# Kernel optimization log

Hardware: AMD Instinct MI355X
Metric: run time of the kernel (lower is better)

Reference implementation:

```python
import jax, jax.numpy as jnp
import numpy as np

DIM = 128      # d_msa
HEADS = 8
DH = 64        # dim_head
INNER = HEADS * DH  # 512
R = 64         # tie_attn_dim (MSA rows)
N = 512        # residues
DPAIR = 128
LN_EPS = 1e-5


def _layernorm(x, g, b):
    mu = jnp.mean(x, axis=-1, keepdims=True)
    var = jnp.mean((x - mu) ** 2, axis=-1, keepdims=True)
    return (x - mu) * jax.lax.rsqrt(var + LN_EPS) * g + b


def setup_inputs() -> dict:
    key = jax.random.key(0)
    ks = jax.random.split(key, 12)
    s = 0.02
    return {
        "x": jax.random.normal(ks[0], (R, N, DIM), jnp.float32),
        "pair_bias": jax.random.normal(ks[1], (1, N, N, DPAIR), jnp.float32),
        "Wq": jax.random.normal(ks[2], (DIM, INNER), jnp.float32) * s,
        "Wkv": jax.random.normal(ks[3], (DIM, 2 * INNER), jnp.float32) * s,
        "Wo": jax.random.normal(ks[4], (INNER, DIM), jnp.float32) * s,
        "bo": jnp.zeros((DIM,), jnp.float32),
        "ln_g": jnp.ones((DPAIR,), jnp.float32),
        "ln_b": jnp.zeros((DPAIR,), jnp.float32),
        "Wpair": jax.random.normal(ks[5], (DPAIR, HEADS), jnp.float32) * s,
        "Wsq": jax.random.normal(ks[6], (DIM, DIM), jnp.float32) * s,
        "bsq": jnp.zeros((DIM,), jnp.float32),
        "Wsk": jax.random.normal(ks[7], (DIM, DIM), jnp.float32) * s,
        "bsk": jnp.zeros((DIM,), jnp.float32),
        "tie_attn_dim": R,
    }


def reference(x, pair_bias, Wq, Wkv, Wo, bo, ln_g, ln_b, Wpair, Wsq, bsq, Wsk, bsk, tie_attn_dim):
    r = tie_attn_dim
    br, n, dim = x.shape
    b = br // r
    h, dh = HEADS, DH
    dsw = dim // h  # per-head dim inside PositionalWiseWeight

    # projections: (b*r, n, inner) -> (b, r, h, n, dh)
    q = (x @ Wq).reshape(b, r, n, h, dh).transpose(0, 1, 3, 2, 4)
    kv = x @ Wkv
    k, v = jnp.split(kv, 2, axis=-1)
    k = k.reshape(b, r, n, h, dh).transpose(0, 1, 3, 2, 4)
    v = v.reshape(b, r, n, h, dh).transpose(0, 1, 3, 2, 4)

    # soft tied row weights (PositionalWiseWeight): w[b, i(pos), h, r]
    m = x.reshape(b, r, n, dim)
    sq = (m[:, :1] @ Wsq + bsq).reshape(b, 1, n, h, dsw).transpose(0, 2, 3, 1, 4)  # b n h 1 d
    sk = (m @ Wsk + bsk).reshape(b, r, n, h, dsw).transpose(0, 2, 3, 1, 4)          # b n h r d
    wlog = jnp.einsum('bnhud,bnhrd->bnhr', sq, sk) / np.float32(np.sqrt(dsw))
    w = jax.nn.softmax(wlog, axis=-1)  # softmax over rows r

    # tied-row attention logits with soft weights
    scale = np.float32(dh) ** -0.5
    dots = jnp.einsum('bihr,brhid,brhjd->bhij', w, q, k) * scale

    # pair bias: LayerNorm + Linear(dim_pair -> heads), broadcast into logits
    pb = _layernorm(pair_bias, ln_g, ln_b) @ Wpair  # (b, i, j, h)
    dots = dots + pb.transpose(0, 3, 1, 2)

    attn = jax.nn.softmax(dots, axis=-1)  # (b, h, i, j)

    out = jnp.einsum('bhij,brhjd->brhid', attn, v)           # (b, r, h, n, dh)
    out = out.transpose(0, 1, 3, 2, 4).reshape(br, n, h * dh)
    out = out @ Wo + bo                                       # (b*r, n, dim)
    return out.reshape(1, br, n, dim)
```

## Files before the change

### kernel.cpp

```cpp
#include <hip/hip_runtime.h>
#include <hip/hip_bf16.h>

typedef unsigned short u16;
typedef unsigned int u32;
typedef __attribute__((ext_vector_type(8))) short short8;
typedef __attribute__((ext_vector_type(4))) float floatx4;

__device__ inline float bf2f(u16 u) { union { u32 i; float f; } v; v.i = ((u32)u) << 16; return v.f; }
__device__ inline u16 f2bf(float f) {
    union { float f; u32 i; } v; v.f = f;
    u32 lsb = (v.i >> 16) & 1u;
    v.i += 0x7fffu + lsb;
    return (u16)(v.i >> 16);
}

__device__ inline uint4 pack8(float4 a, float4 b) {
    uint4 q;
    q.x = (u32)f2bf(a.x) | ((u32)f2bf(a.y) << 16);
    q.y = (u32)f2bf(a.z) | ((u32)f2bf(a.w) << 16);
    q.z = (u32)f2bf(b.x) | ((u32)f2bf(b.y) << 16);
    q.w = (u32)f2bf(b.z) | ((u32)f2bf(b.w) << 16);
    return q;
}

__device__ inline void ld8(u16* dst, const float* src) {
    const float4 a = *(const float4*)src;
    const float4 b = *(const float4*)(src + 4);
    *(uint4*)dst = pack8(a, b);
}

__device__ inline void async16(u16* ldst, const u16* gsrc) {
    __builtin_amdgcn_global_load_lds((const __attribute__((address_space(1))) u32*)gsrc,
                                     (__attribute__((address_space(3))) u32*)ldst, 16, 0, 0);
}

template <int N> __device__ inline void waitvm() {
    static_assert(N == 0 || N == 3 || N == 4 || N == 6 || N == 8, "unsupported vmcnt");
    if constexpr (N == 0) asm volatile("s_waitcnt vmcnt(0)" ::: "memory");
    if constexpr (N == 3) asm volatile("s_waitcnt vmcnt(3)" ::: "memory");
    if constexpr (N == 4) asm volatile("s_waitcnt vmcnt(4)" ::: "memory");
    if constexpr (N == 6) asm volatile("s_waitcnt vmcnt(6)" ::: "memory");
    if constexpr (N == 8) asm volatile("s_waitcnt vmcnt(8)" ::: "memory");
}
__device__ inline void barrier_raw() {
    asm volatile("s_barrier" ::: "memory");
    __builtin_amdgcn_sched_barrier(0);
}
__device__ inline void waitlgkm0() {
    asm volatile("s_waitcnt lgkmcnt(0)" ::: "memory");
    __builtin_amdgcn_sched_barrier(0);
}

template <int BM, int BN, class Epi>
__global__ __launch_bounds__(256) void gemm_nt(const u16* __restrict__ A, const u16* __restrict__ B,
                                               long sAz, long sBz, int lda, int ldb, int K, int zlog, Epi epi)
{
    constexpr int AELE = BM * 32, BELE = BN * 32;
    constexpr int SLOT = AELE + BELE;
    constexpr int IA = BM / 64, IB = BN / 64;
    constexpr int PW = IA + IB;
    constexpr bool STAGE = Epi::chunked;
    static_assert(!STAGE || BN == 128, "chunked epilogue assumes BN=128");
    constexpr int LDC = BN + 4;
    constexpr size_t RB = sizeof(u16) * 4 * (size_t)SLOT;
    constexpr size_t EBR = STAGE ? sizeof(float) * 64 * (size_t)LDC : 0;
    constexpr size_t EBV = (STAGE && Epi::kv) ? sizeof(float) * 128 * 68 : 0;
    constexpr size_t EB = EBR > EBV ? EBR : EBV;
    constexpr size_t LB = RB > EB ? RB : EB;
    __shared__ __align__(16) char smem[LB];
    u16* lds = (u16*)smem;
    const int tid  = threadIdx.x;
    const int lane = tid & 63;
    const int wave = tid >> 6;
    const int z    = blockIdx.z;
    const int zh   = z >> zlog;
    const int zk   = z & ((1 << zlog) - 1);
    if constexpr (Epi::ylim >= 0) {
        if (zh != 0 && (int)blockIdx.y >= Epi::ylim) return;
    }
    const long row0 = (long)blockIdx.y * BM;
    const long col0 = (long)blockIdx.x * BN;
    const u16* Ab = A + (long)zh * sAz + row0 * lda + (long)zk * K;
    const u16* Bb = B + (long)zh * sBz + col0 * ldb + (long)zk * K;
    constexpr int WM = BM / 2, WN = BN / 2, TM = WM / 16, TN = WN / 16;
    const int wm = (wave >> 1) * WM;
    const int wn = (wave & 1) * WN;
    const int l15 = lane & 15;
    const int quad = lane >> 4;
    const int swz = (l15 >> 1) & 3;

    floatx4 acc[TM][TN];
#pragma unroll
    for (int i = 0; i < TM; i++)
#pragma unroll
        for (int j = 0; j < TN; j++) acc[i][j] = (floatx4){0.f, 0.f, 0.f, 0.f};

    auto stage = [&](int slot, int ki) {
        const int k0 = ki << 5;
        u16* base = lds + slot * SLOT;
#pragma unroll
        for (int i2 = 0; i2 < IA; i2++) {
            int s = wave * (IA * 64) + i2 * 64 + lane;
            int r = s >> 2, c = (s & 3) ^ ((r >> 1) & 3);
            async16(base + (wave * (IA * 64) + i2 * 64) * 8, Ab + (long)r * lda + k0 + c * 8);
        }
        u16* bbase = base + AELE;
#pragma unroll
        for (int i2 = 0; i2 < IB; i2++) {
            int s = wave * (IB * 64) + i2 * 64 + lane;
            int r = s >> 2, c = (s & 3) ^ ((r >> 1) & 3);
            async16(bbase + (wave * (IB * 64) + i2 * 64) * 8, Bb + (long)r * ldb + k0 + c * 8);
        }
    };

    auto compute = [&](int slot) {
        const u16* As = lds + slot * SLOT;
        const u16* Bs = As + AELE;
        short8 af[TM], bfr[TN];
#pragma unroll
        for (int t = 0; t < TM; t++)
            af[t] = *(const short8*)(As + (wm + t * 16 + l15) * 32 + (quad ^ swz) * 8);
#pragma unroll
        for (int t = 0; t < TN; t++)
            bfr[t] = *(const short8*)(Bs + (wn + t * 16 + l15) * 32 + (quad ^ swz) * 8);
        waitlgkm0();
#pragma unroll
        for (int i = 0; i < TM; i++)
#pragma unroll
            for (int j = 0; j < TN; j++)
                acc[i][j] = __builtin_amdgcn_mfma_f32_16x16x32_bf16(af[i], bfr[j], acc[i][j], 0, 0, 0);
    };

    const int nIter = K >> 5;
    stage(0, 0);
    stage(1, 1);
    for (int i = 0; i + 2 < nIter; i++) {
        stage((i + 2) & 3, i + 2);
        waitvm<2 * PW>();
        barrier_raw();
        compute(i & 3);
    }
    waitvm<PW>(); barrier_raw(); compute((nIter - 2) & 3);
    waitvm<0>();  barrier_raw(); compute((nIter - 1) & 3);

    if constexpr (STAGE) {
        float* cs = (float*)smem;
        constexpr int NP = BM / 64;
        bool vtile = false;
        if constexpr (Epi::kv) vtile = (col0 >= 512);
#pragma unroll
        for (int p = 0; p < NP; p++) {
            __syncthreads();
            if (!vtile) {
                if ((wm >> 6) == p) {
                    const int lr0 = wm & 63;
#pragma unroll
                    for (int i = 0; i < TM; i++)
#pragma unroll
                        for (int j = 0; j < TN; j++)
#pragma unroll
                            for (int r = 0; r < 4; r++)
                                cs[(lr0 + i * 16 + quad * 4 + r) * LDC + wn + j * 16 + l15] = acc[i][j][r];
                }
                __syncthreads();
                constexpr int CPT = (64 * BN) / (256 * 8);
#pragma unroll
                for (int k = 0; k < CPT; k++) {
                    int g = k * 256 + tid;
                    int row = g >> 4, c8 = (g & 15) * 8;
                    const float* pp = cs + row * LDC + c8;
                    float4 a = *(const float4*)pp;
                    float4 b = *(const float4*)(pp + 4);
                    epi.chunk(zh, zk, (int)row0 + p * 64 + row, (int)col0 + c8, a, b);
                }
            }
            if constexpr (Epi::kv) {
                if (vtile) {
                    if ((wm >> 6) == p) {
                        const int lr0 = wm & 63;
#pragma unroll
                        for (int i = 0; i < TM; i++)
#pragma unroll
                            for (int j = 0; j < TN; j++)
                                *(float4*)&cs[(wn + j * 16 + l15) * 68 + lr0 + i * 16 + quad * 4] =
                                    (float4){acc[i][j][0], acc[i][j][1], acc[i][j][2], acc[i][j][3]};
                    }
                    __syncthreads();
#pragma unroll
                    for (int k = 0; k < 4; k++) {
                        int q = k * 256 + tid;
                        int colL = q >> 3, rg = q & 7;
                        const float* pp = cs + colL * 68 + rg * 8;
                        float4 a = *(const float4*)pp;
                        float4 b = *(const float4*)(pp + 4);
                        epi.vchunk(zh, (int)row0 + p * 64 + rg * 8, (int)col0 + colL, a, b);
                    }
                }
            }
        }
    } else {
#pragma unroll
        for (int i = 0; i < TM; i++)
#pragma unroll
            for (int j = 0; j < TN; j++)
#pragma unroll
                for (int r = 0; r < 4; r++) {
                    int row = (int)row0 + wm + i * 16 + quad * 4 + r;
                    int col = (int)col0 + wn + j * 16 + l15;
                    epi(zh, zk, row, col, acc[i][j][r]);
                }
    }
}

struct EpiSkSq {
    static constexpr bool chunked = true;
    static constexpr bool kv = false;
    static constexpr int ylim = 8;
    u16* sk; u16* sq; const float* bsk; const float* bsq;
    __device__ void chunk(int zh, int, int row, int col, float4 a, float4 b) const {
        const float* bias = zh ? bsq : bsk;
        u16* C = zh ? sq : sk;
        const float4* bp = (const float4*)(bias + col);
        float4 b0 = bp[0], b1 = bp[1];
        a.x += b0.x; a.y += b0.y; a.z += b0.z; a.w += b0.w;
        b.x += b1.x; b.y += b1.y; b.z += b1.z; b.w += b1.w;
        *(uint4*)(C + (long)row * 128 + col) = pack8(a, b);
    }
};
struct EpiQ {
    static constexpr bool chunked = true;
    static constexpr bool kv = false;
    static constexpr int ylim = -1;
    u16* Qw; const float* w;
    __device__ void chunk(int, int, int row, int col, float4 a, float4 b) const {
        int r = row >> 9, i = row & 511, h = col >> 6, d = col & 63;
        float s = w[((long)(i * 8 + h)) * 64 + r] * 0.125f;
        a.x *= s; a.y *= s; a.z *= s; a.w *= s;
        b.x *= s; b.y *= s; b.z *= s; b.w *= s;
        *(uint4*)(Qw + (long)h * 2097152 + (long)i * 4096 + r * 64 + d) = pack8(a, b);
    }
};
struct EpiKV {
    static constexpr bool chunked = true;
    static constexpr bool kv = true;
    static constexpr int ylim = -1;
    u16* Kp; u16* Vt;
    __device__ void chunk(int, int, int row, int col, float4 a, float4 b) const {
        int r = row >> 9, j = row & 511;
        int h = col >> 6, d = col & 63;
        *(uint4*)(Kp + (long)h * 2097152 + (long)j * 4096 + r * 64 + d) = pack8(a, b);
    }
    __device__ void vchunk(int, int row8, int col, float4 a, float4 b) const {
        int r = row8 >> 9, j0 = row8 & 511;
        int c = col - 512, h = c >> 6, d = c & 63;
        *(uint4*)(Vt + (long)h * 2097152 + ((long)r * 64 + d) * 512 + j0) = pack8(a, b);
    }
};
struct EpiDotsAtomic {
    static constexpr bool chunked = false;
    static constexpr bool kv = false;
    static constexpr int ylim = -1;
    float* pbdots;
    __device__ void operator()(int zh, int, int row, int col, float v) const {
        atomicAdd(pbdots + (long)zh * 262144 + (long)row * 512 + col, v);
    }
};
struct EpiDotsPart {
    static constexpr bool chunked = false;
    static constexpr bool kv = false;
    static constexpr int ylim = -1;
    float* pbd; float* parts;
    __device__ void operator()(int zh, int zk, int row, int col, float v) const {
        long idx = (long)zh * 262144 + (long)row * 512 + col;
        if (zk == 0) pbd[idx] += v;
        else         parts[(long)(zk - 1) * 2097152 + idx] = v;
    }
};
struct EpiPV {
    static constexpr bool chunked = true;
    static constexpr bool kv = false;
    static constexpr int ylim = -1;
    u16* O2;
    __device__ void chunk(int zh, int, int row, int col, float4 a, float4 b) const {
        int r = col >> 6, d = col & 63;
        *(uint4*)(O2 + ((long)r * 512 + row) * 512 + zh * 64 + d) = pack8(a, b);
    }
};
struct EpiOut {
    static constexpr bool chunked = true;
    static constexpr bool kv = false;
    static constexpr int ylim = -1;
    float* out; const float* bo;
    __device__ void chunk(int, int, int row, int col, float4 a, float4 b) const {
        const float4* bp = (const float4*)(bo + col);
        float4 b0 = bp[0], b1 = bp[1];
        a.x += b0.x; a.y += b0.y; a.z += b0.z; a.w += b0.w;
        b.x += b1.x; b.y += b1.y; b.z += b1.z; b.w += b1.w;
        float4* o = (float4*)(out + (long)row * 128 + col);
        o[0] = a; o[1] = b;
    }
};

__device__ inline void trans_dev(const float* __restrict__ src, u16* __restrict__ dst,
                                 int R, int C, int bx, int by, int tid)
{
    __shared__ u16 t[32][33];
    int c0 = bx * 32, r0 = by * 32;
    int tx = tid & 31, ty = tid >> 5;
#pragma unroll
    for (int i = 0; i < 32; i += 8) t[ty + i][tx] = f2bf(src[(long)(r0 + ty + i) * C + c0 + tx]);
    __syncthreads();
#pragma unroll
    for (int i = 0; i < 32; i += 8) dst[(long)(c0 + ty + i) * R + r0 + tx] = t[tx][ty + i];
}

__global__ __launch_bounds__(256) void prep_kernel(
    const float* __restrict__ x, u16* __restrict__ xbf,
    const float* __restrict__ Wq, u16* __restrict__ WqT,
    const float* __restrict__ Wkv, u16* __restrict__ WkvT,
    const float* __restrict__ Wsk, u16* __restrict__ WskT,
    const float* __restrict__ Wsq, u16* __restrict__ WsqT,
    const float* __restrict__ Wo, u16* __restrict__ WoT,
    const float* __restrict__ g, const float* __restrict__ b,
    const float* __restrict__ Wp, float* __restrict__ Wg, float* __restrict__ SB)
{
    int gb = blockIdx.x, tid = threadIdx.x;
    if (gb < 2048) { long i = ((long)gb * 256 + tid) * 8; ld8(xbf + i, x + i); return; }
    gb -= 2048;
    if (gb < 64)  { trans_dev(Wq,  WqT,  128, 512,  gb & 15, gb >> 4, tid); return; }
    gb -= 64;
    if (gb < 128) { trans_dev(Wkv, WkvT, 128, 1024, gb & 31, gb >> 5, tid); return; }
    gb -= 128;
    if (gb < 16)  { trans_dev(Wsk, WskT, 128, 128,  gb & 3,  gb >> 2, tid); return; }
    gb -= 16;
    if (gb < 16)  { trans_dev(Wsq, WsqT, 128, 128,  gb & 3,  gb >> 2, tid); return; }
    gb -= 16;
    if (gb < 64)  { trans_dev(Wo,  WoT,  512, 128,  gb & 3,  gb >> 2, tid); return; }
    for (int t = tid; t < 1024; t += 256) Wg[t] = g[t >> 3] * Wp[t];
    if (tid < 16) {
        int h = tid & 7;
        const float* src = (tid < 8) ? g : b;
        float s = 0.f;
        for (int c = 0; c < 128; c++) s += src[c] * Wp[c * 8 + h];
        SB[tid] = s;
    }
}

__global__ __launch_bounds__(256) void rowweight_kernel(const u16* __restrict__ sk, const u16* __restrict__ sq,
                                                        float* __restrict__ w)
{
    int wid = blockIdx.x * 4 + (threadIdx.x >> 6);
    int lane = threadIdx.x & 63;
    int i = wid >> 3, h = wid & 7;
    const u16* sqp = sq + i * 128 + h * 16;
    const u16* skp = sk + ((long)lane * 512 + i) * 128 + h * 16;
    float dot = 0.f;
#pragma unroll
    for (int c = 0; c < 16; c++) dot += bf2f(sqp[c]) * bf2f(skp[c]);
    float logit = dot * 0.25f;
    float m = logit;
#pragma unroll
    for (int o = 32; o > 0; o >>= 1) m = fmaxf(m, __shfl_xor(m, o));
    float e = __expf(logit - m);
    float ssum = e;
#pragma unroll
    for (int o = 32; o > 0; o >>= 1) ssum += __shfl_xor(ssum, o);
    w[(long)wid * 64 + lane] = e / ssum;
}

__global__ __launch_bounds__(256) void pb_kernel(const float* __restrict__ pair, const float* __restrict__ Wg,
                                                 const float* __restrict__ SB, float* __restrict__ pb)
{
    __shared__ __align__(16) float Ls[64 * 132];
    __shared__ float sWg[1024];
    __shared__ float sSB[16];
    int tid = threadIdx.x;
    for (int t = tid; t < 1024; t += 256) sWg[t] = Wg[t];
    if (tid < 16) sSB[tid] = SB[tid];
    long base = (long)blockIdx.x * 8192;
    const float4* src = (const float4*)(pair + base);
#pragma unroll
    for (int k = 0; k < 8; k++) {
        int e = tid + k * 256;
        float4 v = src[e];
        int r = e >> 5, c = (e & 31) << 2;
        *(float4*)(&Ls[r * 132 + c]) = v;
    }
    __syncthreads();
    int r = tid >> 2, sub = tid & 3;
    const float* row = &Ls[r * 132];
    float sum = 0.f, sqs = 0.f;
#pragma unroll
    for (int k = 0; k < 8; k++) {
        float4 v = *(const float4*)(&row[sub * 32 + k * 4]);
        sum += v.x + v.y + v.z + v.w;
        sqs += v.x * v.x + v.y * v.y + v.z * v.z + v.w * v.w;
    }
    sum += __shfl_xor(sum, 1); sqs += __shfl_xor(sqs, 1);
    sum += __shfl_xor(sum, 2); sqs += __shfl_xor(sqs, 2);
    float mu = sum * (1.f / 128.f);
    float var = sqs * (1.f / 128.f) - mu * mu;
    float rstd = rsqrtf(var + 1e-5f);
    int h0 = sub * 2;
    float a0 = 0.f, a1 = 0.f;
#pragma unroll
    for (int k = 0; k < 32; k++) {
        float4 v = *(const float4*)(&row[k * 4]);
        int c = k * 4;
        a0 += v.x * sWg[c * 8 + h0]     + v.y * sWg[(c + 1) * 8 + h0]
            + v.z * sWg[(c + 2) * 8 + h0] + v.w * sWg[(c + 3) * 8 + h0];
        a1 += v.x * sWg[c * 8 + h0 + 1]     + v.y * sWg[(c + 1) * 8 + h0 + 1]
            + v.z * sWg[(c + 2) * 8 + h0 + 1] + v.w * sWg[(c + 3) * 8 + h0 + 1];
    }
    long idx = (long)blockIdx.x * 64 + r;
    pb[(long)h0 * 262144 + idx]       = rstd * (a0 - mu * sSB[h0])     + sSB[8 + h0];
    pb[(long)(h0 + 1) * 262144 + idx] = rstd * (a1 - mu * sSB[h0 + 1]) + sSB[8 + h0 + 1];
}

__global__ __launch_bounds__(256) void softmax_kernel(const float* __restrict__ dots,
                                                      const float* __restrict__ parts, int np,
                                                      u16* __restrict__ attn)
{
    int row = blockIdx.x * 4 + (threadIdx.x >> 6);
    int lane = threadIdx.x & 63;
    long base = (long)row * 512;
    const float* dp = dots + base;
    float v[8];
#pragma unroll
    for (int k = 0; k < 8; k++) v[k] = dp[k * 64 + lane];
    for (int t = 0; t < np; t++) {
        const float* pp = parts + (long)t * 2097152 + base;
#pragma unroll
        for (int k = 0; k < 8; k++) v[k] += pp[k * 64 + lane];
    }
    float m = v[0];
#pragma unroll
    for (int k = 1; k < 8; k++) m = fmaxf(m, v[k]);
#pragma unroll
    for (int o = 32; o > 0; o >>= 1) m = fmaxf(m, __shfl_xor(m, o));
    float s = 0.f;
#pragma unroll
    for (int k = 0; k < 8; k++) { v[k] = __expf(v[k] - m); s += v[k]; }
#pragma unroll
    for (int o = 32; o > 0; o >>= 1) s += __shfl_xor(s, o);
    float inv = 1.f / s;
    u16* ap = attn + (long)row * 512;
#pragma unroll
    for (int k = 0; k < 8; k++) ap[k * 64 + lane] = f2bf(v[k] * inv);
}

extern "C" void kernel_launch(void* const* d_in, const int* in_sizes, int n_in,
                              void* d_out, int out_size, void* d_ws, size_t ws_size,
                              hipStream_t stream)
{
    const float* x    = (const float*)d_in[0];
    const float* pair = (const float*)d_in[1];
    const float* Wq   = (const float*)d_in[2];
    const float* Wkv  = (const float*)d_in[3];
    const float* Wo   = (const float*)d_in[4];
    const float* bo   = (const float*)d_in[5];
    const float* lng  = (const float*)d_in[6];
    const float* lnb  = (const float*)d_in[7];
    const float* Wp   = (const float*)d_in[8];
    const float* Wsq  = (const float*)d_in[9];
    const float* bsq  = (const float*)d_in[10];
    const float* Wsk  = (const float*)d_in[11];
    const float* bsk  = (const float*)d_in[12];
    float* out = (float*)d_out;

    char* ws = (char*)d_ws;
    size_t off = 0;
    auto alloc = [&](size_t bytes) -> char* {
        char* p = ws + off; off += (bytes + 255) & ~(size_t)255; return p;
    };
    u16* WqT  = (u16*)alloc(512 * 128 * 2);
    u16* WkvT = (u16*)alloc(1024 * 128 * 2);
    u16* WskT = (u16*)alloc(128 * 128 * 2);
    u16* WsqT = (u16*)alloc(128 * 128 * 2);
    u16* WoT  = (u16*)alloc(128 * 512 * 2);
    u16* xbf  = (u16*)alloc((size_t)32768 * 128 * 2);
    u16* sk   = (u16*)alloc((size_t)32768 * 128 * 2);
    u16* sq   = (u16*)alloc(512 * 128 * 2);
    float* w  = (float*)alloc((size_t)4096 * 64 * 4);
    float* Wg = (float*)alloc(1024 * 4);
    float* SB = (float*)alloc(16 * 4);
    u16* bufA = (u16*)alloc((size_t)8 * 512 * 4096 * 2);
    u16* bufB = (u16*)alloc((size_t)8 * 512 * 4096 * 2);
    u16* Vt   = (u16*)alloc((size_t)8 * 4096 * 512 * 2);
    float* pbd = (float*)alloc((size_t)8 * 512 * 512 * 4);
    float* parts = (float*)alloc((size_t)3 * 2097152 * 4);
    const bool useParts = (off <= ws_size);
    u16* attn = sk;

    dim3 blk(256);

    prep_kernel<<<dim3(2337), blk, 0, stream>>>(x, xbf, Wq, WqT, Wkv, WkvT,
                                                Wsk, WskT, Wsq, WsqT, Wo, WoT,
                                                lng, lnb, Wp, Wg, SB);

    gemm_nt<64, 128, EpiSkSq><<<dim3(1, 512, 2), blk, 0, stream>>>(
        xbf, WskT, 0, 16384, 128, 128, 128, 0, EpiSkSq{sk, sq, bsk, bsq});
    rowweight_kernel<<<dim3(1024), blk, 0, stream>>>(sk, sq, w);

    gemm_nt<128, 128, EpiKV><<<dim3(8, 256, 1), blk, 0, stream>>>(
        xbf, WkvT, 0, 0, 128, 128, 128, 0, EpiKV{bufB, Vt});

    pb_kernel<<<dim3(4096), blk, 0, stream>>>(pair, Wg, SB, pbd);

    gemm_nt<128, 128, EpiQ><<<dim3(4, 256, 1), blk, 0, stream>>>(
        xbf, WqT, 0, 0, 128, 128, 128, 0, EpiQ{bufA, w});

    if (useParts) {
        gemm_nt<128, 128, EpiDotsPart><<<dim3(4, 4, 32), blk, 0, stream>>>(
            bufA, bufB, 2097152, 2097152, 4096, 4096, 1024, 2, EpiDotsPart{pbd, parts});
        softmax_kernel<<<dim3(1024), blk, 0, stream>>>(pbd, parts, 3, attn);
    } else {
        gemm_nt<128, 128, EpiDotsAtomic><<<dim3(4, 4, 64), blk, 0, stream>>>(
            bufA, bufB, 2097152, 2097152, 4096, 4096, 512, 3, EpiDotsAtomic{pbd});
        softmax_kernel<<<dim3(1024), blk, 0, stream>>>(pbd, pbd, 0, attn);
    }

    gemm_nt<128, 128, EpiPV><<<dim3(32, 4, 8), blk, 0, stream>>>(
        attn, Vt, 262144, 2097152, 512, 512, 512, 0, EpiPV{bufB});

    gemm_nt<64, 128, EpiOut><<<dim3(1, 512, 1), blk, 0, stream>>>(
        bufB, WoT, 0, 0, 512, 512, 512, 0, EpiOut{out, bo});
}
```

Before: 392.9 us.

## Fuse Q and KV projections, use 3-slot LDS pipeline, vectorize dots epilogue

Merges the separate Q and KV projection GEMMs into one launch with a combined epilogue that routes columns to scaled Q, K, or transposed V buffers. This cuts a kernel launch and rereads of x. The GEMM main loop drops from four LDS slots to three, waiting and barriering before issuing the next stage, which lowers LDS footprint and may raise occupancy but leaves less prefetch slack. The split-K dots epilogue now goes through the staged chunk path, so pbd and the partial buffers are written with float4 vector stores. The fused launch assumes WkvT sits directly after WqT in memory.

```diff
diff --git a/kernel.cpp b/kernel.cpp
--- a/kernel.cpp
+++ b/kernel.cpp
@@ -35,8 +35,9 @@
 }
 
 template <int N> __device__ inline void waitvm() {
-    static_assert(N == 0 || N == 3 || N == 4 || N == 6 || N == 8, "unsupported vmcnt");
+    static_assert(N == 0 || N == 2 || N == 3 || N == 4 || N == 6 || N == 8, "unsupported vmcnt");
     if constexpr (N == 0) asm volatile("s_waitcnt vmcnt(0)" ::: "memory");
+    if constexpr (N == 2) asm volatile("s_waitcnt vmcnt(2)" ::: "memory");
     if constexpr (N == 3) asm volatile("s_waitcnt vmcnt(3)" ::: "memory");
     if constexpr (N == 4) asm volatile("s_waitcnt vmcnt(4)" ::: "memory");
     if constexpr (N == 6) asm volatile("s_waitcnt vmcnt(6)" ::: "memory");
@@ -62,7 +63,7 @@
     constexpr bool STAGE = Epi::chunked;
     static_assert(!STAGE || BN == 128, "chunked epilogue assumes BN=128");
     constexpr int LDC = BN + 4;
-    constexpr size_t RB = sizeof(u16) * 4 * (size_t)SLOT;
+    constexpr size_t RB = sizeof(u16) * 3 * (size_t)SLOT;
     constexpr size_t EBR = STAGE ? sizeof(float) * 64 * (size_t)LDC : 0;
     constexpr size_t EBV = (STAGE && Epi::kv) ? sizeof(float) * 128 * 68 : 0;
     constexpr size_t EB = EBR > EBV ? EBR : EBV;
@@ -134,20 +135,22 @@
     const int nIter = K >> 5;
     stage(0, 0);
     stage(1, 1);
+    int s0 = 0, s1 = 1, s2 = 2;
     for (int i = 0; i + 2 < nIter; i++) {
-        stage((i + 2) & 3, i + 2);
-        waitvm<2 * PW>();
+        waitvm<PW>();
         barrier_raw();
-        compute(i & 3);
-    }
-    waitvm<PW>(); barrier_raw(); compute((nIter - 2) & 3);
-    waitvm<0>();  barrier_raw(); compute((nIter - 1) & 3);
+        stage(s2, i + 2);
+        compute(s0);
+        int t = s0; s0 = s1; s1 = s2; s2 = t;
+    }
+    waitvm<PW>(); barrier_raw(); compute(s0);
+    waitvm<0>();  barrier_raw(); compute(s1);
 
     if constexpr (STAGE) {
         float* cs = (float*)smem;
         constexpr int NP = BM / 64;
         bool vtile = false;
-        if constexpr (Epi::kv) vtile = (col0 >= 512);
+        if constexpr (Epi::kv) vtile = (col0 >= Epi::vbase);
 #pragma unroll
         for (int p = 0; p < NP; p++) {
             __syncthreads();
@@ -215,6 +218,7 @@
 struct EpiSkSq {
     static constexpr bool chunked = true;
     static constexpr bool kv = false;
+    static constexpr int vbase = 0;
     static constexpr int ylim = 8;
     u16* sk; u16* sq; const float* bsk; const float* bsq;
     __device__ void chunk(int zh, int, int row, int col, float4 a, float4 b) const {
@@ -227,38 +231,35 @@
         *(uint4*)(C + (long)row * 128 + col) = pack8(a, b);
     }
 };
-struct EpiQ {
-    static constexpr bool chunked = true;
-    static constexpr bool kv = false;
-    static constexpr int ylim = -1;
-    u16* Qw; const float* w;
-    __device__ void chunk(int, int, int row, int col, float4 a, float4 b) const {
-        int r = row >> 9, i = row & 511, h = col >> 6, d = col & 63;
-        float s = w[((long)(i * 8 + h)) * 64 + r] * 0.125f;
-        a.x *= s; a.y *= s; a.z *= s; a.w *= s;
-        b.x *= s; b.y *= s; b.z *= s; b.w *= s;
-        *(uint4*)(Qw + (long)h * 2097152 + (long)i * 4096 + r * 64 + d) = pack8(a, b);
-    }
-};
-struct EpiKV {
+struct EpiQKV {
     static constexpr bool chunked = true;
     static constexpr bool kv = true;
+    static constexpr int vbase = 1024;
     static constexpr int ylim = -1;
-    u16* Kp; u16* Vt;
+    u16* Qw; u16* Kp; u16* Vt; const float* w;
     __device__ void chunk(int, int, int row, int col, float4 a, float4 b) const {
-        int r = row >> 9, j = row & 511;
-        int h = col >> 6, d = col & 63;
-        *(uint4*)(Kp + (long)h * 2097152 + (long)j * 4096 + r * 64 + d) = pack8(a, b);
+        int r = row >> 9, i = row & 511;
+        if (col < 512) {
+            int h = col >> 6, d = col & 63;
+            float s = w[((long)(i * 8 + h)) * 64 + r] * 0.125f;
+            a.x *= s; a.y *= s; a.z *= s; a.w *= s;
+            b.x *= s; b.y *= s; b.z *= s; b.w *= s;
+            *(uint4*)(Qw + (long)h * 2097152 + (long)i * 4096 + r * 64 + d) = pack8(a, b);
+        } else {
+            int c = col - 512, h = c >> 6, d = c & 63;
+            *(uint4*)(Kp + (long)h * 2097152 + (long)i * 4096 + r * 64 + d) = pack8(a, b);
+        }
     }
     __device__ void vchunk(int, int row8, int col, float4 a, float4 b) const {
         int r = row8 >> 9, j0 = row8 & 511;
-        int c = col - 512, h = c >> 6, d = c & 63;
+        int c = col - vbase, h = c >> 6, d = c & 63;
         *(uint4*)(Vt + (long)h * 2097152 + ((long)r * 64 + d) * 512 + j0) = pack8(a, b);
     }
 };
 struct EpiDotsAtomic {
     static constexpr bool chunked = false;
     static constexpr bool kv = false;
+    static constexpr int vbase = 0;
     static constexpr int ylim = -1;
     float* pbdots;
     __device__ void operator()(int zh, int, int row, int col, float v) const {
@@ -266,19 +267,29 @@
     }
 };
 struct EpiDotsPart {
-    static constexpr bool chunked = false;
+    static constexpr bool chunked = true;
     static constexpr bool kv = false;
+    static constexpr int vbase = 0;
     static constexpr int ylim = -1;
     float* pbd; float* parts;
-    __device__ void operator()(int zh, int zk, int row, int col, float v) const {
+    __device__ void chunk(int zh, int zk, int row, int col, float4 a, float4 b) const {
         long idx = (long)zh * 262144 + (long)row * 512 + col;
-        if (zk == 0) pbd[idx] += v;
-        else         parts[(long)(zk - 1) * 2097152 + idx] = v;
+        if (zk == 0) {
+            float4* p = (float4*)(pbd + idx);
+            float4 p0 = p[0], p1 = p[1];
+            p0.x += a.x; p0.y += a.y; p0.z += a.z; p0.w += a.w;
+            p1.x += b.x; p1.y += b.y; p1.z += b.z; p1.w += b.w;
+            p[0] = p0; p[1] = p1;
+        } else {
+            float4* p = (float4*)(parts + (long)(zk - 1) * 2097152 + idx);
+            p[0] = a; p[1] = b;
+        }
     }
 };
 struct EpiPV {
     static constexpr bool chunked = true;
     static constexpr bool kv = false;
+    static constexpr int vbase = 0;
     static constexpr int ylim = -1;
     u16* O2;
     __device__ void chunk(int zh, int, int row, int col, float4 a, float4 b) const {
@@ -289,6 +300,7 @@
 struct EpiOut {
     static constexpr bool chunked = true;
     static constexpr bool kv = false;
+    static constexpr int vbase = 0;
     static constexpr int ylim = -1;
     float* out; const float* bo;
     __device__ void chunk(int, int, int row, int col, float4 a, float4 b) const {
@@ -502,13 +514,10 @@
         xbf, WskT, 0, 16384, 128, 128, 128, 0, EpiSkSq{sk, sq, bsk, bsq});
     rowweight_kernel<<<dim3(1024), blk, 0, stream>>>(sk, sq, w);
 
-    gemm_nt<128, 128, EpiKV><<<dim3(8, 256, 1), blk, 0, stream>>>(
-        xbf, WkvT, 0, 0, 128, 128, 128, 0, EpiKV{bufB, Vt});
-
     pb_kernel<<<dim3(4096), blk, 0, stream>>>(pair, Wg, SB, pbd);
 
-    gemm_nt<128, 128, EpiQ><<<dim3(4, 256, 1), blk, 0, stream>>>(
-        xbf, WqT, 0, 0, 128, 128, 128, 0, EpiQ{bufA, w});
+    gemm_nt<128, 128, EpiQKV><<<dim3(12, 256, 1), blk, 0, stream>>>(
+        xbf, WqT, 0, 0, 128, 128, 128, 0, EpiQKV{bufA, bufB, Vt, w});
 
     if (useParts) {
         gemm_nt<128, 128, EpiDotsPart><<<dim3(4, 4, 32), blk, 0, stream>>>(
```

Result: faster. 364.9 us (-7.1%).
